# Optimization experiments

Measured on AMD Instinct MI355X. Metric: run time of the kernel, lower is better.

The kernel has to match this reference:

```python
import jax, jax.numpy as jnp
import numpy as np

N = 4096      # total nodes
G = 8         # num graphs
NPG = 512     # nodes per graph
F = 128       # num_features
H = 128       # hidden_dim (mlp_layers=1 -> single Linear)
E = 131072    # num edges
ALPHA = 0.5


def setup_inputs() -> dict:
    key = jax.random.key(0)
    k1, k2, k3, k4 = jax.random.split(key, 4)
    x = jax.random.normal(k1, (N, F), dtype=jnp.float32)
    batch = (jnp.arange(N) // NPG).astype(jnp.int32)  # sorted graph ids
    # edges constrained within graphs (as to_dense_adj assumes)
    src = jax.random.randint(k2, (E,), 0, N)
    off = (src // NPG) * NPG
    dst = off + jax.random.randint(k3, (E,), 0, NPG)
    edge_index = jnp.stack([src, dst]).astype(jnp.int32)
    W0 = jax.random.normal(k4, (H, F), dtype=jnp.float32) / np.float32(np.sqrt(F))
    b0 = jnp.zeros((H,), dtype=jnp.float32)
    prob = jnp.array([0.5], dtype=jnp.float32)
    return {"x": x, "W0": W0, "b0": b0, "prob": prob,
            "edge_index": edge_index, "batch": batch}


def reference(x, W0, b0, prob, edge_index, batch):
    # MLP (num_layers==1): single Linear
    X_hat = x @ W0.T + b0                               # [N, H]
    # similarity, normalized by squared Frobenius norm (torch.norm(X_hat)**2)
    S = (X_hat @ X_hat.T) / jnp.sum(X_hat * X_hat)      # [N, N]

    # to_dense_adj(edge_index, batch, max_num_nodes=N): per-graph LOCAL-indexed
    # dense adjacency padded to N (faithfully reproduces the original indexing).
    counts = jax.ops.segment_sum(jnp.ones((N,), jnp.float32), batch, num_segments=G)
    offsets = jnp.concatenate([jnp.zeros((1,), jnp.int32),
                               jnp.cumsum(counts.astype(jnp.int32))[:-1]])
    src, dst = edge_index[0], edge_index[1]
    g = batch[src]
    lu = src - offsets[g]
    lv = dst - offsets[batch[dst]]
    A = jnp.zeros((G, N, N), jnp.float32).at[g, lu, lv].add(1.0)  # [G, N, N]

    # In the loop, graph g uses A[g] with the GLOBAL graph-g block mask:
    # row i of graph batch[i] -> gather A[batch[i], i, :]
    A_sel = A[batch, jnp.arange(N)]                     # [N, N]
    block = (batch[:, None] == batch[None, :]).astype(jnp.float32)
    # Z = relu(S - prob + alpha * A) masked to same-graph blocks
    Wmat = jax.nn.relu(S - prob[0] + ALPHA * A_sel) * block  # [N, N]

    # sparse extraction: nonzeros of Wmat are (rewired_edge_index, edge_weights);
    # return the dense weight matrix (same information, fixed shape).
    edge_ratio = jnp.count_nonzero(Wmat).astype(jnp.float32) / np.float32(E)
    return Wmat, edge_ratio, prob
```

## Files before the change

kernel.cpp:

```cpp
#include <hip/hip_runtime.h>


#define NN   4096
#define GG   8
#define NPG  512
#define FF   128
#define HH   128
#define NE   131072
#define ALPHA 0.5f

typedef short v8s __attribute__((ext_vector_type(8)));
typedef float v4f __attribute__((ext_vector_type(4)));

#define ACNT_BYTES ((size_t)NPG * NPG * 4)
#define NORMP_OFF  (ACNT_BYTES + 64)
#define NORMS_OFF  (ACNT_BYTES + 576)
#define XH_OFF     (ACNT_BYTES + 4096)
#define XHB_OFF    (XH_OFF + (size_t)NN * HH * 4)

static __device__ __forceinline__ unsigned short f2bf(float f) {
    union { float f; unsigned u; } v; v.f = f;
    unsigned r = v.u + 0x7FFFu + ((v.u >> 16) & 1u);
    return (unsigned short)(r >> 16);
}

__global__ __launch_bounds__(256) void k_prep(const float* __restrict__ x,
                                              const float* __restrict__ W0,
                                              const float* __restrict__ b0,
                                              float* __restrict__ Xh,
                                              unsigned short* __restrict__ Xhb,
                                              float* __restrict__ normp,
                                              int* __restrict__ Acnt,
                                              float* __restrict__ out) {
    int bx = blockIdx.x;
    int tid = threadIdx.x;

    if (bx >= 128) {
        int zb = bx - 128;
        if (zb == 0 && tid == 0) {
            out[(size_t)NN * NN]     = 0.f;
            out[(size_t)NN * NN + 1] = 0.f;
        }
        float4 z = make_float4(0.f, 0.f, 0.f, 0.f);
        float4* a4 = (float4*)Acnt;
#pragma unroll
        for (int k = 0; k < 4; ++k) a4[(size_t)zb * 1024 + tid + k * 256] = z;
        return;
    }

    __shared__ float As[16][68];
    __shared__ float Bs[16][68];
    __shared__ float red[256];

    int tm = bx >> 1, tn = bx & 1;
    int r0 = tm * 64, j0 = tn * 64;
    int tx = tid & 15, ty = tid >> 4;
    int li = tid & 63, kq = tid >> 6;

    float acc[4][4];
#pragma unroll
    for (int i = 0; i < 4; ++i)
#pragma unroll
        for (int j = 0; j < 4; ++j) acc[i][j] = 0.f;

    for (int k0 = 0; k0 < FF; k0 += 16) {
        float4 av = *(const float4*)&x [(size_t)(r0 + li) * FF + k0 + kq * 4];
        float4 bv = *(const float4*)&W0[(size_t)(j0 + li) * FF + k0 + kq * 4];
        As[kq*4+0][li] = av.x; As[kq*4+1][li] = av.y;
        As[kq*4+2][li] = av.z; As[kq*4+3][li] = av.w;
        Bs[kq*4+0][li] = bv.x; Bs[kq*4+1][li] = bv.y;
        Bs[kq*4+2][li] = bv.z; Bs[kq*4+3][li] = bv.w;
        __syncthreads();
#pragma unroll
        for (int k = 0; k < 16; ++k) {
            float4 a = *(const float4*)&As[k][ty * 4];
            float4 b = *(const float4*)&Bs[k][tx * 4];
            float ar[4] = {a.x, a.y, a.z, a.w};
            float br[4] = {b.x, b.y, b.z, b.w};
#pragma unroll
            for (int i = 0; i < 4; ++i)
#pragma unroll
                for (int j = 0; j < 4; ++j) acc[i][j] += ar[i] * br[j];
        }
        __syncthreads();
    }

    float4 bb = *(const float4*)&b0[j0 + tx * 4];
    float ss = 0.f;
#pragma unroll
    for (int ii = 0; ii < 4; ++ii) {
        int row = r0 + ty * 4 + ii;
        float4 v;
        v.x = acc[ii][0] + bb.x;
        v.y = acc[ii][1] + bb.y;
        v.z = acc[ii][2] + bb.z;
        v.w = acc[ii][3] + bb.w;
        *(float4*)&Xh[(size_t)row * HH + j0 + tx * 4] = v;
        ushort4 h;
        h.x = f2bf(v.x); h.y = f2bf(v.y); h.z = f2bf(v.z); h.w = f2bf(v.w);
        *(ushort4*)&Xhb[(size_t)row * HH + j0 + tx * 4] = h;
        ss += v.x * v.x + v.y * v.y + v.z * v.z + v.w * v.w;
    }

    red[tid] = ss;
    __syncthreads();
    for (int s = 128; s > 0; s >>= 1) {
        if (tid < s) red[tid] += red[tid + s];
        __syncthreads();
    }
    if (tid == 0) normp[bx] = red[0];
}

__global__ __launch_bounds__(256) void k_scatter(const int* __restrict__ ei,
                                                 int* __restrict__ Acnt,
                                                 const float* __restrict__ normp,
                                                 float* __restrict__ normsq) {
    int bx = blockIdx.x;
    int tid = threadIdx.x;
    if (bx == 512) {
        __shared__ float red[128];
        if (tid < 128) red[tid] = normp[tid];
        __syncthreads();
        for (int s = 64; s > 0; s >>= 1) {
            if (tid < s) red[tid] += red[tid + s];
            __syncthreads();
        }
        if (tid == 0) *normsq = red[0];
        return;
    }
    int e = bx * 256 + tid;
    int src = ei[e], dst = ei[NE + e];
    if ((unsigned)src < (unsigned)NPG && (unsigned)dst < (unsigned)NPG)
        atomicAdd(&Acnt[src * NPG + dst], 1);
}

__global__ __launch_bounds__(256) void k_diag(const unsigned short* __restrict__ Xhb,
                                              const int* __restrict__ Acnt,
                                              const float* __restrict__ normsq,
                                              const float* __restrict__ prob,
                                              float* __restrict__ out) {
    __shared__ int s_cnt[4];

    int bt = blockIdx.x;
    int tid = threadIdx.x;
    int gb = bt >> 6;
    int t  = bt & 63;
    int tm = t >> 3, tn = t & 7;
    int r0 = gb * NPG + tm * 64, c0 = gb * NPG + tn * 64;
    int lane = tid & 63, w = tid >> 6;
    int m = lane & 15, quad = lane >> 4;
    int koff = quad * 8;

    const unsigned short* arow = &Xhb[(size_t)(r0 + w * 16 + m) * HH];

    v4f acc[4];
#pragma unroll
    for (int ct = 0; ct < 4; ++ct) acc[ct] = (v4f){0.f, 0.f, 0.f, 0.f};

#pragma unroll
    for (int k0 = 0; k0 < HH; k0 += 32) {
        v8s a = *(const v8s*)&arow[k0 + koff];
#pragma unroll
        for (int ct = 0; ct < 4; ++ct) {
            v8s b = *(const v8s*)&Xhb[(size_t)(c0 + ct * 16 + m) * HH + k0 + koff];
            acc[ct] = __builtin_amdgcn_mfma_f32_16x16x32_bf16(a, b, acc[ct], 0, 0, 0);
        }
    }

    float inv = 1.0f / (*normsq);
    float p = prob[0];
    int cnt = 0;
#pragma unroll
    for (int ct = 0; ct < 4; ++ct) {
#pragma unroll
        for (int reg = 0; reg < 4; ++reg) {
            int row = r0 + w * 16 + quad * 4 + reg;
            int col = c0 + ct * 16 + m;
            float s = acc[ct][reg] * inv;
            float a = (gb == 0) ? (float)Acnt[row * NPG + col] : 0.f;
            float pre = s - p + ALPHA * a;
            out[(size_t)row * NN + col] = pre > 0.f ? pre : 0.f;
            cnt += (pre > 0.f) ? 1 : 0;
        }
    }

#pragma unroll
    for (int off = 32; off > 0; off >>= 1) cnt += __shfl_down(cnt, off);
    if (lane == 0) s_cnt[w] = cnt;
    __syncthreads();
    if (tid == 0) {
        int total = s_cnt[0] + s_cnt[1] + s_cnt[2] + s_cnt[3];
        atomicAdd(&out[(size_t)NN * NN], (float)total / (float)NE);
        if (bt == 0) out[(size_t)NN * NN + 1] = prob[0];
    }
}

extern "C" void kernel_launch(void* const* d_in, const int* in_sizes, int n_in,
                              void* d_out, int out_size, void* d_ws, size_t ws_size,
                              hipStream_t stream) {
    (void)in_sizes; (void)n_in; (void)out_size; (void)ws_size;
    const float* x    = (const float*)d_in[0];
    const float* W0   = (const float*)d_in[1];
    const float* b0   = (const float*)d_in[2];
    const float* prob = (const float*)d_in[3];
    const int*   ei   = (const int*)d_in[4];
    float* out = (float*)d_out;
    char*  ws  = (char*)d_ws;

    int*            Acnt   = (int*)ws;
    float*          normp  = (float*)(ws + NORMP_OFF);
    float*          normsq = (float*)(ws + NORMS_OFF);
    float*          Xh     = (float*)(ws + XH_OFF);
    unsigned short* Xhb    = (unsigned short*)(ws + XHB_OFF);

    k_prep<<<192, 256, 0, stream>>>(x, W0, b0, Xh, Xhb, normp, Acnt, out);
    k_scatter<<<513, 256, 0, stream>>>(ei, Acnt, normp, normsq);
    k_diag<<<512, 256, 0, stream>>>(Xhb, Acnt, normsq, prob, out);
}
```

Measured before the change: 106.0 us.

## Move projection GEMM to bf16 MFMA and fuse it with edge scatter

Replaces the fp32 shared-memory SIMT GEMM for X@W0^T with a bf16 MFMA GEMM. x and W0 are cast to bf16 in a new first kernel, which also zeroes the adjacency counts. The projection now runs in the same launch as the edge scatter, and the squared norm is accumulated with atomics, which removes the separate norm-partials reduction and the fp32 Xh store. This cuts scalar FMA work and one stage of reduction. In exchange, X_hat and its Frobenius norm are now computed from bf16 inputs, and the atomic float sum makes the norm order-dependent.

```diff
diff --git a/kernel.cpp b/kernel.cpp
--- a/kernel.cpp
+++ b/kernel.cpp
@@ -13,125 +13,115 @@
 typedef float v4f __attribute__((ext_vector_type(4)));
 
 #define ACNT_BYTES ((size_t)NPG * NPG * 4)
-#define NORMP_OFF  (ACNT_BYTES + 64)
 #define NORMS_OFF  (ACNT_BYTES + 576)
-#define XH_OFF     (ACNT_BYTES + 4096)
-#define XHB_OFF    (XH_OFF + (size_t)NN * HH * 4)
+#define XB_OFF     (ACNT_BYTES + 4096)
+#define W0B_OFF    (XB_OFF + (size_t)NN * FF * 2)
+#define XHB_OFF    (W0B_OFF + 65536)
 
 static __device__ __forceinline__ unsigned short f2bf(float f) {
     union { float f; unsigned u; } v; v.f = f;
     unsigned r = v.u + 0x7FFFu + ((v.u >> 16) & 1u);
     return (unsigned short)(r >> 16);
 }
-
-__global__ __launch_bounds__(256) void k_prep(const float* __restrict__ x,
+static __device__ __forceinline__ ushort4 f2bf4(float4 v) {
+    ushort4 h;
+    h.x = f2bf(v.x); h.y = f2bf(v.y); h.z = f2bf(v.z); h.w = f2bf(v.w);
+    return h;
+}
+
+__global__ __launch_bounds__(256) void k_cast(const float* __restrict__ x,
                                               const float* __restrict__ W0,
-                                              const float* __restrict__ b0,
-                                              float* __restrict__ Xh,
-                                              unsigned short* __restrict__ Xhb,
-                                              float* __restrict__ normp,
+                                              unsigned short* __restrict__ xb,
+                                              unsigned short* __restrict__ W0b,
                                               int* __restrict__ Acnt,
+                                              float* __restrict__ normsq,
                                               float* __restrict__ out) {
     int bx = blockIdx.x;
     int tid = threadIdx.x;
 
-    if (bx >= 128) {
-        int zb = bx - 128;
-        if (zb == 0 && tid == 0) {
+    if (bx < 64) {
+        const float4* x4 = (const float4*)x;
+        ushort4* o4 = (ushort4*)xb;
+        int base = bx * 2048 + tid;
+#pragma unroll
+        for (int k = 0; k < 8; ++k) o4[base + k * 256] = f2bf4(x4[base + k * 256]);
+        return;
+    }
+    if (bx == 64) {
+        const float4* w4 = (const float4*)W0;
+        ushort4* o4 = (ushort4*)W0b;
+#pragma unroll
+        for (int k = 0; k < 16; ++k) o4[tid + k * 256] = f2bf4(w4[tid + k * 256]);
+        if (tid == 0) {
+            *normsq = 0.f;
             out[(size_t)NN * NN]     = 0.f;
             out[(size_t)NN * NN + 1] = 0.f;
         }
-        float4 z = make_float4(0.f, 0.f, 0.f, 0.f);
-        float4* a4 = (float4*)Acnt;
-#pragma unroll
-        for (int k = 0; k < 4; ++k) a4[(size_t)zb * 1024 + tid + k * 256] = z;
         return;
     }
-
-    __shared__ float As[16][68];
-    __shared__ float Bs[16][68];
-    __shared__ float red[256];
-
-    int tm = bx >> 1, tn = bx & 1;
-    int r0 = tm * 64, j0 = tn * 64;
-    int tx = tid & 15, ty = tid >> 4;
-    int li = tid & 63, kq = tid >> 6;
-
-    float acc[4][4];
-#pragma unroll
-    for (int i = 0; i < 4; ++i)
-#pragma unroll
-        for (int j = 0; j < 4; ++j) acc[i][j] = 0.f;
-
-    for (int k0 = 0; k0 < FF; k0 += 16) {
-        float4 av = *(const float4*)&x [(size_t)(r0 + li) * FF + k0 + kq * 4];
-        float4 bv = *(const float4*)&W0[(size_t)(j0 + li) * FF + k0 + kq * 4];
-        As[kq*4+0][li] = av.x; As[kq*4+1][li] = av.y;
-        As[kq*4+2][li] = av.z; As[kq*4+3][li] = av.w;
-        Bs[kq*4+0][li] = bv.x; Bs[kq*4+1][li] = bv.y;
-        Bs[kq*4+2][li] = bv.z; Bs[kq*4+3][li] = bv.w;
-        __syncthreads();
-#pragma unroll
-        for (int k = 0; k < 16; ++k) {
-            float4 a = *(const float4*)&As[k][ty * 4];
-            float4 b = *(const float4*)&Bs[k][tx * 4];
-            float ar[4] = {a.x, a.y, a.z, a.w};
-            float br[4] = {b.x, b.y, b.z, b.w};
-#pragma unroll
-            for (int i = 0; i < 4; ++i)
-#pragma unroll
-                for (int j = 0; j < 4; ++j) acc[i][j] += ar[i] * br[j];
-        }
-        __syncthreads();
-    }
-
-    float4 bb = *(const float4*)&b0[j0 + tx * 4];
-    float ss = 0.f;
-#pragma unroll
-    for (int ii = 0; ii < 4; ++ii) {
-        int row = r0 + ty * 4 + ii;
-        float4 v;
-        v.x = acc[ii][0] + bb.x;
-        v.y = acc[ii][1] + bb.y;
-        v.z = acc[ii][2] + bb.z;
-        v.w = acc[ii][3] + bb.w;
-        *(float4*)&Xh[(size_t)row * HH + j0 + tx * 4] = v;
-        ushort4 h;
-        h.x = f2bf(v.x); h.y = f2bf(v.y); h.z = f2bf(v.z); h.w = f2bf(v.w);
-        *(ushort4*)&Xhb[(size_t)row * HH + j0 + tx * 4] = h;
-        ss += v.x * v.x + v.y * v.y + v.z * v.z + v.w * v.w;
-    }
-
-    red[tid] = ss;
-    __syncthreads();
-    for (int s = 128; s > 0; s >>= 1) {
-        if (tid < s) red[tid] += red[tid + s];
-        __syncthreads();
-    }
-    if (tid == 0) normp[bx] = red[0];
-}
-
-__global__ __launch_bounds__(256) void k_scatter(const int* __restrict__ ei,
-                                                 int* __restrict__ Acnt,
-                                                 const float* __restrict__ normp,
-                                                 float* __restrict__ normsq) {
+    int zb = bx - 65;
+    float4 z = make_float4(0.f, 0.f, 0.f, 0.f);
+    float4* a4 = (float4*)Acnt;
+#pragma unroll
+    for (int k = 0; k < 4; ++k) a4[(size_t)zb * 1024 + tid + k * 256] = z;
+}
+
+__global__ __launch_bounds__(256) void k_mid(const int* __restrict__ ei,
+                                             int* __restrict__ Acnt,
+                                             const unsigned short* __restrict__ xb,
+                                             const unsigned short* __restrict__ W0b,
+                                             const float* __restrict__ b0,
+                                             unsigned short* __restrict__ Xhb,
+                                             float* __restrict__ normsq) {
     int bx = blockIdx.x;
     int tid = threadIdx.x;
-    if (bx == 512) {
-        __shared__ float red[128];
-        if (tid < 128) red[tid] = normp[tid];
-        __syncthreads();
-        for (int s = 64; s > 0; s >>= 1) {
-            if (tid < s) red[tid] += red[tid + s];
-            __syncthreads();
-        }
-        if (tid == 0) *normsq = red[0];
+
+    if (bx < 512) {
+        int e = bx * 256 + tid;
+        int src = ei[e], dst = ei[NE + e];
+        if ((unsigned)src < (unsigned)NPG && (unsigned)dst < (unsigned)NPG)
+            atomicAdd(&Acnt[src * NPG + dst], 1);
         return;
     }
-    int e = bx * 256 + tid;
-    int src = ei[e], dst = ei[NE + e];
-    if ((unsigned)src < (unsigned)NPG && (unsigned)dst < (unsigned)NPG)
-        atomicAdd(&Acnt[src * NPG + dst], 1);
+
+    int b = bx - 512;
+    int lane = tid & 63, w = tid >> 6;
+    int m = lane & 15, quad = lane >> 4;
+    int koff = quad * 8;
+    int r0 = b * 32 + (w >> 1) * 16;
+    int cb = (w & 1) * 64;
+
+    const unsigned short* arow = &xb[(size_t)(r0 + m) * FF];
+
+    v4f acc[4];
+#pragma unroll
+    for (int ct = 0; ct < 4; ++ct) acc[ct] = (v4f){0.f, 0.f, 0.f, 0.f};
+
+#pragma unroll
+    for (int k0 = 0; k0 < FF; k0 += 32) {
+        v8s a = *(const v8s*)&arow[k0 + koff];
+#pragma unroll
+        for (int ct = 0; ct < 4; ++ct) {
+            v8s bf = *(const v8s*)&W0b[(size_t)(cb + ct * 16 + m) * FF + k0 + koff];
+            acc[ct] = __builtin_amdgcn_mfma_f32_16x16x32_bf16(a, bf, acc[ct], 0, 0, 0);
+        }
+    }
+
+    float ss = 0.f;
+#pragma unroll
+    for (int ct = 0; ct < 4; ++ct) {
+#pragma unroll
+        for (int reg = 0; reg < 4; ++reg) {
+            int row = r0 + quad * 4 + reg;
+            int col = cb + ct * 16 + m;
+            float v = acc[ct][reg] + b0[col];
+            Xhb[(size_t)row * HH + col] = f2bf(v);
+            ss += v * v;
+        }
+    }
+#pragma unroll
+    for (int off = 32; off > 0; off >>= 1) ss += __shfl_down(ss, off);
+    if (lane == 0) atomicAdd(normsq, ss);
 }
 
 __global__ __launch_bounds__(256) void k_diag(const unsigned short* __restrict__ Xhb,
@@ -208,12 +198,12 @@
     char*  ws  = (char*)d_ws;
 
     int*            Acnt   = (int*)ws;
-    float*          normp  = (float*)(ws + NORMP_OFF);
     float*          normsq = (float*)(ws + NORMS_OFF);
-    float*          Xh     = (float*)(ws + XH_OFF);
+    unsigned short* xb     = (unsigned short*)(ws + XB_OFF);
+    unsigned short* W0b    = (unsigned short*)(ws + W0B_OFF);
     unsigned short* Xhb    = (unsigned short*)(ws + XHB_OFF);
 
-    k_prep<<<192, 256, 0, stream>>>(x, W0, b0, Xh, Xhb, normp, Acnt, out);
-    k_scatter<<<513, 256, 0, stream>>>(ei, Acnt, normp, normsq);
+    k_cast<<<129, 256, 0, stream>>>(x, W0, xb, W0b, Acnt, normsq, out);
+    k_mid<<<640, 256, 0, stream>>>(ei, Acnt, xb, W0b, b0, Xhb, normsq);
     k_diag<<<512, 256, 0, stream>>>(Xhb, Acnt, normsq, prob, out);
 }
```

Result: no change. 107.9 us (+1.8%).
